# Kernel optimization log

Hardware: AMD Instinct MI355X
Metric: run time of the kernel (lower is better)

The kernel has to match this reference:

```python
import jax, jax.numpy as jnp
import numpy as np

IN_DIM = 128
OUT_DIM = 128
BATCH = 1024
K = 3        # spline order
INIT_G = 3   # initial number of grid intervals


def setup_inputs() -> dict:
    key = jax.random.key(0)
    k1, k2 = jax.random.split(key)
    x = jax.random.normal(k1, (BATCH, IN_DIM), dtype=jnp.float32)
    # grid as in __init__: arange(-k, G+k+1)*h + (-1), tiled per (in,out) edge
    h = (1.0 - (-1.0)) / INIT_G
    grid_row = jnp.arange(-K, INIT_G + K + 1, dtype=jnp.float32) * h - 1.0  # (G+2k+1,) = (10,)
    grid = jnp.tile(grid_row[None, :], (IN_DIM * OUT_DIM, 1))               # (E, 10)
    n_basis = grid.shape[1] - 1 - K                                          # 6
    c_basis = 0.1 * jax.random.normal(k2, (IN_DIM * OUT_DIM, n_basis), dtype=jnp.float32)
    c_spl = jnp.ones(IN_DIM * OUT_DIM, dtype=jnp.float32)
    c_res = jnp.ones(IN_DIM * OUT_DIM, dtype=jnp.float32)
    return {"x": x, "grid": grid, "c_basis": c_basis, "c_spl": c_spl, "c_res": c_res}


def get_spline_basis(x_ext, grid, k=K):
    # x_ext: (E, B), grid: (E, G)
    g = grid[:, :, None]      # (E, G, 1)
    x = x_ext[:, None, :]     # (E, 1, B)
    b = ((x >= g[:, :-1]) & (x < g[:, 1:])).astype(x_ext.dtype)  # (E, G-1, B)
    for KK in range(1, k + 1):  # Cox-de Boor recursion; k is a small static constant
        left = (x - g[:, :-(KK + 1)]) / (g[:, KK:-1] - g[:, :-(KK + 1)])
        right = (g[:, KK + 1:] - x) / (g[:, KK + 1:] - g[:, 1:-KK])
        b = left * b[:, :-1] + right * b[:, 1:]
    return b  # (E, G-1-k, B)


def reference(x, grid, c_basis, c_spl, c_res):
    batch, in_dim = x.shape
    out_dim = c_spl.shape[0] // in_dim
    # broadcast each input feature to every output: edge index = o*in_dim + i
    x_ext = jnp.broadcast_to(x[:, None, :], (batch, out_dim, in_dim)).reshape(batch, in_dim * out_dim).T  # (E, B)
    res = jax.nn.swish(x_ext).T                                  # (B, E) residual activation
    Bi = get_spline_basis(x_ext, grid, K)                        # (E, 6, B)
    spl = jnp.einsum('ej,ejb->eb', c_basis, Bi).T                # (B, E)
    y = c_spl[None, :] * spl + c_res[None, :] * res              # (B, E)
    y = y.reshape(batch, out_dim, in_dim).sum(axis=2) / in_dim   # (B, out_dim)
    grid_r = grid.reshape(out_dim, in_dim, -1)
    input_norm = grid_r[:, :, -1] - grid_r[:, :, 0] + 1e-05      # (out, in)
    spl_reg = jnp.mean(jnp.abs(spl.reshape(batch, out_dim, in_dim)), axis=0) / input_norm
    return (y, spl_reg)
```

## Files before the change

kernel.cpp:

```cpp
#include <hip/hip_runtime.h>

static constexpr int BATCH   = 1024;
static constexpr int IN_DIM  = 128;
static constexpr int OUT_DIM = 128;
static constexpr int NEDGE   = IN_DIM * OUT_DIM;
static constexpr int Y_SIZE  = BATCH * OUT_DIM;

static constexpr size_t P_OFF  = 0;
static constexpr size_t P2_OFF = (size_t)NEDGE * 4;

__device__ __forceinline__ void eval_basis(
    float xv, const float* tg, const float* inv1, const float* inv2,
    const float* inv3, float* bb )
{
#pragma unroll
    for (int m = 0; m < 9; ++m)
        bb[m] = (xv >= tg[m] && xv < tg[m + 1]) ? 1.0f : 0.0f;
#pragma unroll
    for (int m = 0; m < 8; ++m)
        bb[m] = (xv - tg[m]) * inv1[m] * bb[m]
              + (tg[m + 2] - xv) * inv1[m + 1] * bb[m + 1];
#pragma unroll
    for (int m = 0; m < 7; ++m)
        bb[m] = (xv - tg[m]) * inv2[m] * bb[m]
              + (tg[m + 3] - xv) * inv2[m + 1] * bb[m + 1];
#pragma unroll
    for (int m = 0; m < 6; ++m)
        bb[m] = (xv - tg[m]) * inv3[m] * bb[m]
              + (tg[m + 4] - xv) * inv3[m + 1] * bb[m + 1];
}

__global__ __launch_bounds__(256) void k_fused(
    const float* __restrict__ x, const float* __restrict__ grid,
    const float* __restrict__ c_basis, const float* __restrict__ c_spl,
    const float* __restrict__ c_res, float* __restrict__ ws)
{
    __shared__ float4 smem4[4096];
    const int t   = threadIdx.x;
    const int blk = blockIdx.x;

    float tg[10];
#pragma unroll
    for (int m = 0; m < 10; ++m) tg[m] = grid[m];
    float inv1[9], inv2[8], inv3[7];
#pragma unroll
    for (int m = 0; m < 9; ++m) inv1[m] = 1.0f / (tg[m + 1] - tg[m]);
#pragma unroll
    for (int m = 0; m < 8; ++m) inv2[m] = 1.0f / (tg[m + 2] - tg[m]);
#pragma unroll
    for (int m = 0; m < 7; ++m) inv3[m] = 1.0f / (tg[m + 3] - tg[m]);

    if (blk < 256) {
        const int bt = blk >> 4;
        const int ot = (blk >> 3) & 1;
        const int ic = blk & 7;
        const int b0 = bt * 64, o0 = ot * 64, i0 = ic * 16;
        float4* Fl = smem4;
        float4* Wl = smem4 + 2048;

        const int bl  = t & 63;
        const int iig = t >> 6;
        const int oo  = t >> 2;
#pragma unroll
        for (int k = 0; k < 4; ++k) {
            const int   ii = iig + 4 * k;
            const float xv = x[(size_t)(b0 + bl) * IN_DIM + i0 + ii];
            float bb[9];
            eval_basis(xv, tg, inv1, inv2, inv3, bb);
            const float sw = xv / (1.0f + expf(-xv));
            const int xr = (bl >> 2) & 1;
            Fl[ii * 128 + ((bl * 2)     ^ xr)] = make_float4(bb[0], bb[1], bb[2], bb[3]);
            Fl[ii * 128 + ((bl * 2 + 1) ^ xr)] = make_float4(bb[4], bb[5], sw, 0.f);

            const int iw = (t & 3) + 4 * k;
            const int e  = (o0 + oo) * IN_DIM + i0 + iw;
            const float cs = c_spl[e];
            const float cr = c_res[e];
            const float* cb = c_basis + (size_t)e * 6;
            const int xw = ((oo >> 2) & 3) << 1;
            Wl[oo * 32 + ((iw * 2)     ^ xw)] =
                make_float4(cs * cb[0], cs * cb[1], cs * cb[2], cs * cb[3]);
            Wl[oo * 32 + ((iw * 2 + 1) ^ xw)] =
                make_float4(cs * cb[4], cs * cb[5], cr, 0.f);
        }
        __syncthreads();

        const int bi = t & 15;
        const int og = t >> 4;
        float acc[4][4];
#pragma unroll
        for (int c = 0; c < 4; ++c)
#pragma unroll
            for (int q = 0; q < 4; ++q) acc[c][q] = 0.f;

#pragma unroll 2
        for (int ii = 0; ii < 16; ++ii) {
            float4 fb[4][2], wo[4][2];
#pragma unroll
            for (int c = 0; c < 4; ++c) {
                const int b  = bi + 16 * c;
                const int xr = (b >> 2) & 1;
                fb[c][0] = Fl[ii * 128 + ((b * 2)     ^ xr)];
                fb[c][1] = Fl[ii * 128 + ((b * 2 + 1) ^ xr)];
            }
#pragma unroll
            for (int q = 0; q < 4; ++q) {
                const int o  = og * 4 + q;
                const int xr = (og & 3) << 1;
                wo[q][0] = Wl[o * 32 + ((ii * 2)     ^ xr)];
                wo[q][1] = Wl[o * 32 + ((ii * 2 + 1) ^ xr)];
            }
#pragma unroll
            for (int c = 0; c < 4; ++c)
#pragma unroll
                for (int q = 0; q < 4; ++q) {
                    acc[c][q] += fb[c][0].x * wo[q][0].x + fb[c][0].y * wo[q][0].y
                               + fb[c][0].z * wo[q][0].z + fb[c][0].w * wo[q][0].w
                               + fb[c][1].x * wo[q][1].x + fb[c][1].y * wo[q][1].y
                               + fb[c][1].z * wo[q][1].z + fb[c][1].w * wo[q][1].w;
                }
        }

        float4* P2 = reinterpret_cast<float4*>(ws + P2_OFF);
#pragma unroll
        for (int c = 0; c < 4; ++c)
            P2[((size_t)ic * Y_SIZE
                + (size_t)(b0 + bi + 16 * c) * OUT_DIM + o0 + og * 4) >> 2] =
                make_float4(acc[c][0], acc[c][1], acc[c][2], acc[c][3]);
    } else {
        float4* Flds    = smem4;
        float*  partial = reinterpret_cast<float*>(smem4 + 512);
        const int rb = blk - 256;
        const int i  = rb >> 2;
        const int bq = rb & 3;

        const float xv = x[(size_t)(bq * 256 + t) * IN_DIM + i];
        float bb[9];
        eval_basis(xv, tg, inv1, inv2, inv3, bb);
        Flds[t * 2]     = make_float4(bb[0], bb[1], bb[2], bb[3]);
        Flds[t * 2 + 1] = make_float4(bb[4], bb[5], 0.f, 0.f);

        const int o  = t & 127;
        const int bh = t >> 7;
        const int e  = (o << 7) + i;
        const float* cb = c_basis + (size_t)e * 6;
        const float4 w0 = make_float4(cb[0], cb[1], cb[2], cb[3]);
        const float w1x = cb[4], w1y = cb[5];
        __syncthreads();

        const float4* fl = &Flds[bh * 256];
        float acc = 0.f;
#pragma unroll 4
        for (int bl = 0; bl < 128; ++bl) {
            const float4 f0 = fl[bl * 2 + 0];
            const float4 f1 = fl[bl * 2 + 1];
            const float spl = f0.x * w0.x + f0.y * w0.y + f0.z * w0.z + f0.w * w0.w
                            + f1.x * w1x + f1.y * w1y;
            acc += fabsf(spl);
        }
        partial[t] = acc;
        __syncthreads();
        if (t < 128)
            ws[P_OFF + ((size_t)((t & 127) << 7) + i) * 4 + bq] =
                partial[t] + partial[t + 128];
    }
}

__global__ __launch_bounds__(256) void k_final(
    const float* __restrict__ ws, const float* __restrict__ grid,
    float* __restrict__ out)
{
    const int t   = threadIdx.x;
    const int blk = blockIdx.x;
    if (blk < 128) {
        const int gid = blk * 256 + t;
        const float4* P2 = reinterpret_cast<const float4*>(ws + P2_OFF);
        float4 s = P2[gid];
#pragma unroll
        for (int ic = 1; ic < 8; ++ic) {
            const float4 p = P2[(size_t)ic * (Y_SIZE / 4) + gid];
            s.x += p.x; s.y += p.y; s.z += p.z; s.w += p.w;
        }
        const float sc = 1.0f / (float)IN_DIM;
        reinterpret_cast<float4*>(out)[gid] =
            make_float4(s.x * sc, s.y * sc, s.z * sc, s.w * sc);
    } else {
        const int e = (blk - 128) * 256 + t;
        const float4 p = reinterpret_cast<const float4*>(ws + P_OFF)[e];
        const float invfac = 1.0f / ((float)BATCH * (grid[9] - grid[0] + 1e-5f));
        out[Y_SIZE + e] = (p.x + p.y + p.z + p.w) * invfac;
    }
}

extern "C" void kernel_launch(void* const* d_in, const int* in_sizes, int n_in,
                              void* d_out, int out_size, void* d_ws, size_t ws_size,
                              hipStream_t stream)
{
    const float* x  = (const float*)d_in[0];
    const float* gr = (const float*)d_in[1];
    const float* cb = (const float*)d_in[2];
    const float* cs = (const float*)d_in[3];
    const float* cr = (const float*)d_in[4];
    float* out = (float*)d_out;
    float* ws  = (float*)d_ws;

    k_fused<<<768, 256, 0, stream>>>(x, gr, cb, cs, cr, ws);
    k_final<<<192, 256, 0, stream>>>(ws, gr, out);
}
```

Measured before the change: 80.90 us.

## Split matmul input chunks finer and register-tile the regularizer blocks

The main GEMM-like path now gives each block 8 input features instead of 16. That doubles the number of such blocks to 512, halves their shared memory, and produces 16 partial sums per output that k_final must reduce. The regularizer blocks stage c_basis in shared memory. Each thread now computes 4 outputs over 32 batch rows, and partials are reduced through a padded array, so the basis loads from shared memory are reused across outputs. The aim is more parallelism and occupancy on the 256-CU device, at the cost of extra workspace traffic for partial sums and a longer final reduction.

```diff
diff --git a/kernel.cpp b/kernel.cpp
--- a/kernel.cpp
+++ b/kernel.cpp
@@ -35,7 +35,7 @@
     const float* __restrict__ c_basis, const float* __restrict__ c_spl,
     const float* __restrict__ c_res, float* __restrict__ ws)
 {
-    __shared__ float4 smem4[4096];
+    __shared__ float4 smem4[2048];
     const int t   = threadIdx.x;
     const int blk = blockIdx.x;
 
@@ -50,20 +50,20 @@
 #pragma unroll
     for (int m = 0; m < 7; ++m) inv3[m] = 1.0f / (tg[m + 3] - tg[m]);
 
-    if (blk < 256) {
-        const int bt = blk >> 4;
-        const int ot = (blk >> 3) & 1;
-        const int ic = blk & 7;
-        const int b0 = bt * 64, o0 = ot * 64, i0 = ic * 16;
+    if (blk < 512) {
+        const int bt = blk >> 5;
+        const int ot = (blk >> 4) & 1;
+        const int ic = blk & 15;
+        const int b0 = bt * 64, o0 = ot * 64, i0 = ic * 8;
         float4* Fl = smem4;
-        float4* Wl = smem4 + 2048;
+        float4* Wl = smem4 + 1024;
 
         const int bl  = t & 63;
         const int iig = t >> 6;
         const int oo  = t >> 2;
 #pragma unroll
-        for (int k = 0; k < 4; ++k) {
-            const int   ii = iig + 4 * k;
+        for (int k = 0; k < 2; ++k) {
+            const int   ii = iig * 2 + k;
             const float xv = x[(size_t)(b0 + bl) * IN_DIM + i0 + ii];
             float bb[9];
             eval_basis(xv, tg, inv1, inv2, inv3, bb);
@@ -72,21 +72,21 @@
             Fl[ii * 128 + ((bl * 2)     ^ xr)] = make_float4(bb[0], bb[1], bb[2], bb[3]);
             Fl[ii * 128 + ((bl * 2 + 1) ^ xr)] = make_float4(bb[4], bb[5], sw, 0.f);
 
-            const int iw = (t & 3) + 4 * k;
+            const int iw = (t & 3) * 2 + k;
             const int e  = (o0 + oo) * IN_DIM + i0 + iw;
             const float cs = c_spl[e];
             const float cr = c_res[e];
             const float* cb = c_basis + (size_t)e * 6;
             const int xw = ((oo >> 2) & 3) << 1;
-            Wl[oo * 32 + ((iw * 2)     ^ xw)] =
+            Wl[oo * 16 + ((iw * 2)     ^ xw)] =
                 make_float4(cs * cb[0], cs * cb[1], cs * cb[2], cs * cb[3]);
-            Wl[oo * 32 + ((iw * 2 + 1) ^ xw)] =
+            Wl[oo * 16 + ((iw * 2 + 1) ^ xw)] =
                 make_float4(cs * cb[4], cs * cb[5], cr, 0.f);
         }
         __syncthreads();
 
-        const int bi = t & 15;
-        const int og = t >> 4;
+        const int bi  = t & 15;
+        const int og4 = t >> 4;
         float acc[4][4];
 #pragma unroll
         for (int c = 0; c < 4; ++c)
@@ -94,7 +94,7 @@
             for (int q = 0; q < 4; ++q) acc[c][q] = 0.f;
 
 #pragma unroll 2
-        for (int ii = 0; ii < 16; ++ii) {
+        for (int ii = 0; ii < 8; ++ii) {
             float4 fb[4][2], wo[4][2];
 #pragma unroll
             for (int c = 0; c < 4; ++c) {
@@ -105,10 +105,10 @@
             }
 #pragma unroll
             for (int q = 0; q < 4; ++q) {
-                const int o  = og * 4 + q;
-                const int xr = (og & 3) << 1;
-                wo[q][0] = Wl[o * 32 + ((ii * 2)     ^ xr)];
-                wo[q][1] = Wl[o * 32 + ((ii * 2 + 1) ^ xr)];
+                const int o  = og4 * 4 + q;
+                const int xr = (og4 & 3) << 1;
+                wo[q][0] = Wl[o * 16 + ((ii * 2)     ^ xr)];
+                wo[q][1] = Wl[o * 16 + ((ii * 2 + 1) ^ xr)];
             }
 #pragma unroll
             for (int c = 0; c < 4; ++c)
@@ -125,44 +125,62 @@
 #pragma unroll
         for (int c = 0; c < 4; ++c)
             P2[((size_t)ic * Y_SIZE
-                + (size_t)(b0 + bi + 16 * c) * OUT_DIM + o0 + og * 4) >> 2] =
+                + (size_t)(b0 + bi + 16 * c) * OUT_DIM + o0 + og4 * 4) >> 2] =
                 make_float4(acc[c][0], acc[c][1], acc[c][2], acc[c][3]);
     } else {
-        float4* Flds    = smem4;
-        float*  partial = reinterpret_cast<float*>(smem4 + 512);
-        const int rb = blk - 256;
+        float4* Bl  = smem4;
+        float4* CBl = smem4 + 512;
+        float*  partial = reinterpret_cast<float*>(smem4 + 768);
+        const int rb = blk - 512;
         const int i  = rb >> 2;
         const int bq = rb & 3;
 
         const float xv = x[(size_t)(bq * 256 + t) * IN_DIM + i];
         float bb[9];
         eval_basis(xv, tg, inv1, inv2, inv3, bb);
-        Flds[t * 2]     = make_float4(bb[0], bb[1], bb[2], bb[3]);
-        Flds[t * 2 + 1] = make_float4(bb[4], bb[5], 0.f, 0.f);
-
-        const int o  = t & 127;
-        const int bh = t >> 7;
-        const int e  = (o << 7) + i;
-        const float* cb = c_basis + (size_t)e * 6;
-        const float4 w0 = make_float4(cb[0], cb[1], cb[2], cb[3]);
-        const float w1x = cb[4], w1y = cb[5];
+        {
+            const int idx = ((t & 31) * 8 + (t >> 5)) * 2;
+            Bl[idx]     = make_float4(bb[0], bb[1], bb[2], bb[3]);
+            Bl[idx + 1] = make_float4(bb[4], bb[5], 0.f, 0.f);
+        }
+        if (t < 128) {
+            const float* cbp = c_basis + (size_t)(t * IN_DIM + i) * 6;
+            CBl[t * 2]     = make_float4(cbp[0], cbp[1], cbp[2], cbp[3]);
+            CBl[t * 2 + 1] = make_float4(cbp[4], cbp[5], 0.f, 0.f);
+        }
         __syncthreads();
 
-        const float4* fl = &Flds[bh * 256];
-        float acc = 0.f;
+        const int og = t >> 3;
+        const int sl = t & 7;
+        float4 w0[4], w1[4];
+#pragma unroll
+        for (int q = 0; q < 4; ++q) {
+            w0[q] = CBl[(og * 4 + q) * 2];
+            w1[q] = CBl[(og * 4 + q) * 2 + 1];
+        }
+        float acc[4] = {0.f, 0.f, 0.f, 0.f};
 #pragma unroll 4
-        for (int bl = 0; bl < 128; ++bl) {
-            const float4 f0 = fl[bl * 2 + 0];
-            const float4 f1 = fl[bl * 2 + 1];
-            const float spl = f0.x * w0.x + f0.y * w0.y + f0.z * w0.z + f0.w * w0.w
-                            + f1.x * w1x + f1.y * w1y;
-            acc += fabsf(spl);
-        }
-        partial[t] = acc;
+        for (int bl = 0; bl < 32; ++bl) {
+            const float4 f0 = Bl[(bl * 8 + sl) * 2];
+            const float4 f1 = Bl[(bl * 8 + sl) * 2 + 1];
+#pragma unroll
+            for (int q = 0; q < 4; ++q) {
+                const float spl = f0.x * w0[q].x + f0.y * w0[q].y
+                                + f0.z * w0[q].z + f0.w * w0[q].w
+                                + f1.x * w1[q].x + f1.y * w1[q].y;
+                acc[q] += fabsf(spl);
+            }
+        }
+#pragma unroll
+        for (int q = 0; q < 4; ++q)
+            partial[(og * 4 + q) * 9 + sl] = acc[q];
         __syncthreads();
-        if (t < 128)
-            ws[P_OFF + ((size_t)((t & 127) << 7) + i) * 4 + bq] =
-                partial[t] + partial[t + 128];
+        if (t < 128) {
+            float s = 0.f;
+#pragma unroll
+            for (int k = 0; k < 8; ++k) s += partial[t * 9 + k];
+            ws[P_OFF + ((size_t)(t * IN_DIM + i) << 2) + bq] = s;
+        }
     }
 }
 
@@ -177,7 +195,7 @@
         const float4* P2 = reinterpret_cast<const float4*>(ws + P2_OFF);
         float4 s = P2[gid];
 #pragma unroll
-        for (int ic = 1; ic < 8; ++ic) {
+        for (int ic = 1; ic < 16; ++ic) {
             const float4 p = P2[(size_t)ic * (Y_SIZE / 4) + gid];
             s.x += p.x; s.y += p.y; s.z += p.z; s.w += p.w;
         }
@@ -204,6 +222,6 @@
     float* out = (float*)d_out;
     float* ws  = (float*)d_ws;
 
-    k_fused<<<768, 256, 0, stream>>>(x, gr, cb, cs, cr, ws);
+    k_fused<<<1024, 256, 0, stream>>>(x, gr, cb, cs, cr, ws);
     k_final<<<192, 256, 0, stream>>>(ws, gr, out);
 }
```

Result: no change. 80.09 us (-1.0%).
